# Kernel optimization log

Measured on AMD Instinct MI355X. Metric: run time of the kernel, lower is better.

Reference implementation:

```python
import jax, jax.numpy as jnp
import numpy as np

D_MODEL = 4096
D_FF = 16384
TOKENS = 4096
K_SEL = 4096
SCALE = 0.02  # keep activations numerically tame


def setup_inputs() -> dict:
    key = jax.random.key(0)
    ks = jax.random.split(key, 6)
    x = jax.random.normal(ks[0], (TOKENS, D_MODEL), dtype=jnp.float32)
    fc1_w = jax.random.normal(ks[1], (D_FF, D_MODEL), dtype=jnp.float32) * SCALE
    bias1 = jax.random.normal(ks[2], (D_FF,), dtype=jnp.float32) * SCALE
    fc2_w_t = jax.random.normal(ks[3], (D_FF, D_MODEL), dtype=jnp.float32) * SCALE
    bias2 = jax.random.normal(ks[4], (D_MODEL,), dtype=jnp.float32) * SCALE
    index_vec = jnp.sort(jax.random.randint(ks[5], (K_SEL,), 0, D_FF, dtype=jnp.int32))
    return {"x": x, "fc1_w": fc1_w, "bias1": bias1, "fc2_w_t": fc2_w_t,
            "bias2": bias2, "index_vec": index_vec}


def reference(x, fc1_w, bias1, fc2_w_t, bias2, index_vec):
    # gather_matmul_col_h: gather selected neuron rows of fc1, GEMM + bias + relu
    w1 = fc1_w[index_vec]                 # [k, d]
    b1 = bias1[index_vec]                 # [k]
    h = jax.nn.relu(jnp.einsum('td,kd->tk', x, w1) + b1)  # [T, k]
    # gather_matmul_row_h: gather selected rows of fc2^T, GEMM + bias
    w2 = fc2_w_t[index_vec]               # [k, out]
    out = jnp.einsum('tk,ko->to', h, w2) + bias2          # [T, out]
    return out
```

## Files before the change

### kernel.cpp

```cpp
#include <hip/hip_runtime.h>
#include <stdint.h>
#include <type_traits>

#define TOKENS  4096
#define D_MODEL 4096
#define D_FF    16384
#define K_SEL   4096

typedef __attribute__((ext_vector_type(8))) short short8;
typedef __attribute__((ext_vector_type(4))) float float4v;

typedef const __attribute__((address_space(1))) unsigned int* gptr_t;
typedef __attribute__((address_space(3))) unsigned int* lptr_t;

__device__ inline unsigned short f2bf(float f) {
    union { float f; unsigned int u; } v; v.f = f;
    unsigned int r = v.u + 0x7fffu + ((v.u >> 16) & 1u);
    return (unsigned short)(r >> 16);
}

__global__ void gather_cast_kernel(const float* __restrict__ src,
                                   const int* __restrict__ idx,
                                   unsigned short* __restrict__ dst,
                                   int cols) {
    long e = ((long)blockIdx.x * blockDim.x + threadIdx.x) * 8;
    int row = (int)(e / cols);
    int col = (int)(e - (long)row * cols);
    long srow = idx ? (long)idx[row] : (long)row;
    const float4* s = (const float4*)(src + srow * cols + col);
    float4 a = s[0], b = s[1];
    short8 o;
    o[0] = (short)f2bf(a.x); o[1] = (short)f2bf(a.y);
    o[2] = (short)f2bf(a.z); o[3] = (short)f2bf(a.w);
    o[4] = (short)f2bf(b.x); o[5] = (short)f2bf(b.y);
    o[6] = (short)f2bf(b.z); o[7] = (short)f2bf(b.w);
    *(short8*)(dst + e) = o;
}

__global__ void gather_transpose_cast_kernel(const float* __restrict__ src,
                                             const int* __restrict__ idx,
                                             unsigned short* __restrict__ dst,
                                             int srcCols, int rows) {
    __shared__ float tile[32][33];
    int tx = threadIdx.x;
    int ty = threadIdx.y;
    int k0 = blockIdx.x * 32;
    int n0 = blockIdx.y * 32;
#pragma unroll
    for (int r = 0; r < 4; ++r) {
        int k = k0 + ty + r * 8;
        long sr = idx[k];
        tile[ty + r * 8][tx] = src[sr * srcCols + n0 + tx];
    }
    __syncthreads();
#pragma unroll
    for (int r = 0; r < 4; ++r) {
        int n = n0 + ty + r * 8;
        dst[(long)n * rows + k0 + tx] = f2bf(tile[tx][ty + r * 8]);
    }
}

template <int MODE>
__global__ __launch_bounds__(512)
void gemm_nt256(const unsigned short* __restrict__ A,
                const unsigned short* __restrict__ B,
                const float* __restrict__ bias,
                const int* __restrict__ bidx,
                void* __restrict__ Cout,
                int M, int N, int K) {
    extern __shared__ unsigned short lds[];
    unsigned short* AsB = lds;
    unsigned short* BsB = lds + 32768;

    const int tid  = threadIdx.x;
    const int lane = tid & 63;
    const int wave = tid >> 6;
    const int wm   = wave >> 2;
    const int wn   = wave & 3;
    const int quad = lane >> 4;
    const int lr   = lane & 15;

    const int nwg  = (int)(gridDim.x * gridDim.y);
    const int orig = (int)(blockIdx.y * gridDim.x + blockIdx.x);
    const int swz  = (orig & 7) * (nwg >> 3) + (orig >> 3);
    const int bx   = swz % (int)gridDim.x;
    const int by   = swz / (int)gridDim.x;
    const int bm   = by * 256;
    const int bn   = bx * 256;

    const unsigned short* aSrc[2];
    const unsigned short* bSrc[2];
    int ldsOff[2];
#pragma unroll
    for (int i = 0; i < 2; ++i) {
        int p = i * 512 + tid;
        int q = p >> 8, m = p & 255;
        aSrc[i] = A + (long)(bm + m) * K + q * 8;
        bSrc[i] = B + (long)(bn + m) * K + q * 8;
        ldsOff[i] = p * 8;
    }

    float4v acc[8][4];
#pragma unroll
    for (int i = 0; i < 8; ++i)
#pragma unroll
        for (int j = 0; j < 4; ++j)
            acc[i][j] = (float4v)(0.f);

    const int NSUB = K >> 5;

    auto stageA = [&](int s) {
        unsigned short* dst = AsB + (s & 3) * 8192;
#pragma unroll
        for (int i = 0; i < 2; ++i)
            __builtin_amdgcn_global_load_lds((gptr_t)(aSrc[i] + s * 32),
                                             (lptr_t)(dst + ldsOff[i]), 16, 0, 0);
    };
    auto stageB = [&](int s) {
        unsigned short* dst = BsB + (s & 3) * 8192;
#pragma unroll
        for (int i = 0; i < 2; ++i)
            __builtin_amdgcn_global_load_lds((gptr_t)(bSrc[i] + s * 32),
                                             (lptr_t)(dst + ldsOff[i]), 16, 0, 0);
    };

    stageA(0); stageB(0); stageA(1); stageB(1); stageA(2); stageB(2);

    const int rowA = wm * 128 + lr;
    const int rowB = wn * 64 + lr;

    auto kiter = [&](int s, auto waitc, auto dostage) {
        constexpr int  W  = decltype(waitc)::value;
        constexpr bool DS = decltype(dostage)::value;
        if constexpr (W == 8)
            asm volatile("s_waitcnt vmcnt(8)\n\ts_barrier" ::: "memory");
        else if constexpr (W == 4)
            asm volatile("s_waitcnt vmcnt(4)\n\ts_barrier" ::: "memory");
        else
            asm volatile("s_waitcnt vmcnt(0)\n\ts_barrier" ::: "memory");

        const unsigned short* sA = AsB + (s & 3) * 8192;
        const unsigned short* sB = BsB + (s & 3) * 8192;
        const unsigned short* pA = sA + (quad * 256 + rowA) * 8;
        const unsigned short* pB = sB + (quad * 256 + rowB) * 8;

        short8 af[8], bfr[4];
#pragma unroll
        for (int i = 0; i < 4; ++i) af[i] = *(const short8*)(pA + i * 128);
#pragma unroll
        for (int j = 0; j < 4; ++j) bfr[j] = *(const short8*)(pB + j * 128);
        if constexpr (DS) stageA(s + 3);
        __builtin_amdgcn_s_setprio(1);
#pragma unroll
        for (int i = 0; i < 4; ++i)
#pragma unroll
            for (int j = 0; j < 4; ++j)
                acc[i][j] = __builtin_amdgcn_mfma_f32_16x16x32_bf16(
                    af[i], bfr[j], acc[i][j], 0, 0, 0);
        __builtin_amdgcn_s_setprio(0);

#pragma unroll
        for (int i = 0; i < 4; ++i) af[4 + i] = *(const short8*)(pA + 512 + i * 128);
        if constexpr (DS) stageB(s + 3);
        __builtin_amdgcn_s_setprio(1);
#pragma unroll
        for (int i = 4; i < 8; ++i)
#pragma unroll
            for (int j = 0; j < 4; ++j)
                acc[i][j] = __builtin_amdgcn_mfma_f32_16x16x32_bf16(
                    af[i], bfr[j], acc[i][j], 0, 0, 0);
        __builtin_amdgcn_s_setprio(0);
    };

    for (int s = 0; s < NSUB - 3; ++s)
        kiter(s, std::integral_constant<int, 8>{}, std::true_type{});
    kiter(NSUB - 3, std::integral_constant<int, 8>{}, std::false_type{});
    kiter(NSUB - 2, std::integral_constant<int, 4>{}, std::false_type{});
    kiter(NSUB - 1, std::integral_constant<int, 0>{}, std::false_type{});

#pragma unroll
    for (int i = 0; i < 8; ++i) {
        int rowBase = bm + wm * 128 + i * 16 + quad * 4;
#pragma unroll
        for (int j = 0; j < 4; ++j) {
            int col = bn + wn * 64 + j * 16 + lr;
            float bv = (MODE == 1) ? bias[bidx[col]] : bias[col];
#pragma unroll
            for (int r = 0; r < 4; ++r) {
                float v = acc[i][j][r] + bv;
                long off = (long)(rowBase + r) * N + col;
                if (MODE == 1) {
                    v = v > 0.f ? v : 0.f;
                    ((unsigned short*)Cout)[off] = f2bf(v);
                } else {
                    ((float*)Cout)[off] = v;
                }
            }
        }
    }
}

extern "C" void kernel_launch(void* const* d_in, const int* in_sizes, int n_in,
                              void* d_out, int out_size, void* d_ws, size_t ws_size,
                              hipStream_t stream) {
    const float* x      = (const float*)d_in[0];
    const float* fc1_w  = (const float*)d_in[1];
    const float* bias1  = (const float*)d_in[2];
    const float* fc2_wt = (const float*)d_in[3];
    const float* bias2  = (const float*)d_in[4];
    const int*   idx    = (const int*)d_in[5];

    static bool inited = false;
    if (!inited) {
        hipFuncSetAttribute(reinterpret_cast<const void*>(&gemm_nt256<1>),
                            hipFuncAttributeMaxDynamicSharedMemorySize, 131072);
        hipFuncSetAttribute(reinterpret_cast<const void*>(&gemm_nt256<0>),
                            hipFuncAttributeMaxDynamicSharedMemorySize, 131072);
        inited = true;
    }

    char* ws = (char*)d_ws;
    unsigned short* Xb   = (unsigned short*)(ws);
    unsigned short* W1g  = (unsigned short*)(ws + ((size_t)32 << 20));
    unsigned short* W2gT = (unsigned short*)(ws + ((size_t)64 << 20));
    unsigned short* H    = (unsigned short*)(ws + ((size_t)96 << 20));

    gather_cast_kernel<<<(TOKENS * D_MODEL / 8) / 256, 256, 0, stream>>>(
        x, nullptr, Xb, D_MODEL);
    gather_cast_kernel<<<(K_SEL * D_MODEL / 8) / 256, 256, 0, stream>>>(
        fc1_w, idx, W1g, D_MODEL);
    gather_transpose_cast_kernel<<<dim3(K_SEL / 32, D_MODEL / 32), dim3(32, 8), 0, stream>>>(
        fc2_wt, idx, W2gT, D_MODEL, K_SEL);
    gemm_nt256<1><<<dim3(K_SEL / 256, TOKENS / 256), 512, 131072, stream>>>(
        Xb, W1g, bias1, idx, (void*)H, TOKENS, K_SEL, D_MODEL);
    gemm_nt256<0><<<dim3(D_MODEL / 256, TOKENS / 256), 512, 131072, stream>>>(
        H, W2gT, bias2, nullptr, d_out, TOKENS, D_MODEL, K_SEL);
}
```

Before: 851.8 us.

## Restructure GEMM k-loop barriers and widen gather-transpose to 64x64 vector tiles

```diff
diff --git a/kernel.cpp b/kernel.cpp
--- a/kernel.cpp
+++ b/kernel.cpp
@@ -37,26 +37,34 @@
     *(short8*)(dst + e) = o;
 }
 
-__global__ void gather_transpose_cast_kernel(const float* __restrict__ src,
-                                             const int* __restrict__ idx,
-                                             unsigned short* __restrict__ dst,
-                                             int srcCols, int rows) {
-    __shared__ float tile[32][33];
-    int tx = threadIdx.x;
-    int ty = threadIdx.y;
-    int k0 = blockIdx.x * 32;
-    int n0 = blockIdx.y * 32;
-#pragma unroll
-    for (int r = 0; r < 4; ++r) {
-        int k = k0 + ty + r * 8;
-        long sr = idx[k];
-        tile[ty + r * 8][tx] = src[sr * srcCols + n0 + tx];
+__global__ void gather_transpose_cast64(const float* __restrict__ src,
+                                        const int* __restrict__ idx,
+                                        unsigned short* __restrict__ dst,
+                                        int srcCols, int rows) {
+    __shared__ float tile[64][65];
+    int t = threadIdx.x;
+    int k0 = blockIdx.x * 64;
+    int n0 = blockIdx.y * 64;
+    int fr = t >> 4;
+    int fc = (t & 15) * 4;
+#pragma unroll
+    for (int p = 0; p < 4; ++p) {
+        int k = fr + p * 16;
+        long sr = idx[k0 + k];
+        float4 v = *(const float4*)(src + sr * srcCols + n0 + fc);
+        tile[k][fc] = v.x; tile[k][fc + 1] = v.y;
+        tile[k][fc + 2] = v.z; tile[k][fc + 3] = v.w;
     }
     __syncthreads();
 #pragma unroll
-    for (int r = 0; r < 4; ++r) {
-        int n = n0 + ty + r * 8;
-        dst[(long)n * rows + k0 + tx] = f2bf(tile[tx][ty + r * 8]);
+    for (int p = 0; p < 2; ++p) {
+        int n  = (t >> 3) + p * 32;
+        int kc = (t & 7) * 8;
+        short8 o;
+#pragma unroll
+        for (int j = 0; j < 8; ++j)
+            o[j] = (short)f2bf(tile[kc + j][n]);
+        *(short8*)(dst + (long)(n0 + n) * rows + k0 + kc) = o;
     }
 }
 
@@ -125,19 +133,15 @@
     };
 
     stageA(0); stageB(0); stageA(1); stageB(1); stageA(2); stageB(2);
+    asm volatile("s_waitcnt vmcnt(8)" ::: "memory");
+    __builtin_amdgcn_s_barrier();
 
     const int rowA = wm * 128 + lr;
     const int rowB = wn * 64 + lr;
 
-    auto kiter = [&](int s, auto waitc, auto dostage) {
-        constexpr int  W  = decltype(waitc)::value;
+    auto kiter = [&](int s, auto wtrail, auto dostage) {
+        constexpr int  W  = decltype(wtrail)::value;
         constexpr bool DS = decltype(dostage)::value;
-        if constexpr (W == 8)
-            asm volatile("s_waitcnt vmcnt(8)\n\ts_barrier" ::: "memory");
-        else if constexpr (W == 4)
-            asm volatile("s_waitcnt vmcnt(4)\n\ts_barrier" ::: "memory");
-        else
-            asm volatile("s_waitcnt vmcnt(0)\n\ts_barrier" ::: "memory");
 
         const unsigned short* sA = AsB + (s & 3) * 8192;
         const unsigned short* sB = BsB + (s & 3) * 8192;
@@ -145,11 +149,16 @@
         const unsigned short* pB = sB + (quad * 256 + rowB) * 8;
 
         short8 af[8], bfr[4];
+
 #pragma unroll
         for (int i = 0; i < 4; ++i) af[i] = *(const short8*)(pA + i * 128);
 #pragma unroll
         for (int j = 0; j < 4; ++j) bfr[j] = *(const short8*)(pB + j * 128);
         if constexpr (DS) stageA(s + 3);
+        __builtin_amdgcn_sched_barrier(0);
+        __builtin_amdgcn_s_barrier();
+        asm volatile("s_waitcnt lgkmcnt(0)" ::: "memory");
+        __builtin_amdgcn_sched_barrier(0);
         __builtin_amdgcn_s_setprio(1);
 #pragma unroll
         for (int i = 0; i < 4; ++i)
@@ -158,10 +167,16 @@
                 acc[i][j] = __builtin_amdgcn_mfma_f32_16x16x32_bf16(
                     af[i], bfr[j], acc[i][j], 0, 0, 0);
         __builtin_amdgcn_s_setprio(0);
+        __builtin_amdgcn_sched_barrier(0);
+        __builtin_amdgcn_s_barrier();
 
 #pragma unroll
         for (int i = 0; i < 4; ++i) af[4 + i] = *(const short8*)(pA + 512 + i * 128);
         if constexpr (DS) stageB(s + 3);
+        __builtin_amdgcn_sched_barrier(0);
+        __builtin_amdgcn_s_barrier();
+        asm volatile("s_waitcnt lgkmcnt(0)" ::: "memory");
+        __builtin_amdgcn_sched_barrier(0);
         __builtin_amdgcn_s_setprio(1);
 #pragma unroll
         for (int i = 4; i < 8; ++i)
@@ -170,12 +185,20 @@
                 acc[i][j] = __builtin_amdgcn_mfma_f32_16x16x32_bf16(
                     af[i], bfr[j], acc[i][j], 0, 0, 0);
         __builtin_amdgcn_s_setprio(0);
+        __builtin_amdgcn_sched_barrier(0);
+        if constexpr (W == 8)
+            asm volatile("s_waitcnt vmcnt(8)" ::: "memory");
+        else if constexpr (W == 4)
+            asm volatile("s_waitcnt vmcnt(4)" ::: "memory");
+        else
+            asm volatile("s_waitcnt vmcnt(0)" ::: "memory");
+        __builtin_amdgcn_s_barrier();
     };
 
     for (int s = 0; s < NSUB - 3; ++s)
         kiter(s, std::integral_constant<int, 8>{}, std::true_type{});
-    kiter(NSUB - 3, std::integral_constant<int, 8>{}, std::false_type{});
-    kiter(NSUB - 2, std::integral_constant<int, 4>{}, std::false_type{});
+    kiter(NSUB - 3, std::integral_constant<int, 4>{}, std::false_type{});
+    kiter(NSUB - 2, std::integral_constant<int, 0>{}, std::false_type{});
     kiter(NSUB - 1, std::integral_constant<int, 0>{}, std::false_type{});
 
 #pragma unroll
@@ -229,7 +252,7 @@
         x, nullptr, Xb, D_MODEL);
     gather_cast_kernel<<<(K_SEL * D_MODEL / 8) / 256, 256, 0, stream>>>(
         fc1_w, idx, W1g, D_MODEL);
-    gather_transpose_cast_kernel<<<dim3(K_SEL / 32, D_MODEL / 32), dim3(32, 8), 0, stream>>>(
+    gather_transpose_cast64<<<dim3(K_SEL / 64, D_MODEL / 64), 256, 0, stream>>>(
         fc2_wt, idx, W2gT, D_MODEL, K_SEL);
     gemm_nt256<1><<<dim3(K_SEL / 256, TOKENS / 256), 512, 131072, stream>>>(
         Xb, W1g, bias1, idx, (void*)H, TOKENS, K_SEL, D_MODEL);
```

After: 824.0 us. -3.3%, faster.
